# Optimization experiments

Hardware: AMD Instinct MI355X
Metric: run time of the kernel (lower is better)

## Reference

```python
import jax, jax.numpy as jnp
import numpy as np

B, S, E, H, NW, FFN = 16384, 8, 8, 8, 8, 512  # seq==num_heads, embed==n_wires per view() constraint
EPS = 1e-5


def _layer_norm(x, g, b):
    m = x.mean(-1, keepdims=True)
    v = ((x - m) ** 2).mean(-1, keepdims=True)
    return (x - m) / jnp.sqrt(v + EPS) * g + b


def _ring_cnot_z(c):
    # c: [..., NW] = cos(theta) per wire for a product RX state.
    # CNOT(0,1),(1,2),...,(NW-2,NW-1),(NW-1,0) => z_w -> prefix-XOR; Z-expectations factorize:
    # <Z_w> = prod_{j<=w} c_j (w>=1);  <Z_0> = prod_{j>=1} c_j
    cp = jnp.cumprod(c, axis=-1)
    z0 = jnp.prod(c[..., 1:], axis=-1, keepdims=True)
    return jnp.concatenate([z0, cp[..., 1:]], axis=-1)


def setup_inputs() -> dict:
    key = jax.random.key(0)
    ks = jax.random.split(key, 14)
    rn = lambda k, shp, s=0.1: jax.random.normal(k, shp, jnp.float32) * s
    return {
        "x": jax.random.normal(ks[0], (B, S, E), jnp.float32),
        "in_proj_w": rn(ks[1], (3 * E, E)), "in_proj_b": rn(ks[2], (3 * E,)),
        "out_proj_w": rn(ks[3], (E, E)), "out_proj_b": rn(ks[4], (E,)),
        "rx_attn": rn(ks[5], (NW,), 1.0),
        "combine_w": rn(ks[6], (E, E)), "combine_b": rn(ks[7], (E,)),
        "ln1_g": jnp.ones((E,), jnp.float32), "ln1_b": jnp.zeros((E,), jnp.float32),
        "rx_ffn": rn(ks[8], (NW,), 1.0),
        "lin1_w": rn(ks[9], (FFN, NW)), "lin1_b": rn(ks[10], (FFN,)),
        "lin2_w": rn(ks[11], (E, FFN)), "lin2_b": rn(ks[12], (E,)),
        "ln2_g": jnp.ones((E,), jnp.float32), "ln2_b": jnp.zeros((E,), jnp.float32),
    }


def _forward(x, in_proj_w, in_proj_b, out_proj_w, out_proj_b, rx_attn,
             combine_w, combine_b, ln1_g, ln1_b, rx_ffn,
             lin1_w, lin1_b, lin2_w, lin2_b, ln2_g, ln2_b):
    dk = E // H
    # --- nn.MultiheadAttention (self-attn, batch_first, eval/no-dropout) ---
    qkv = x @ in_proj_w.T + in_proj_b                      # [B,S,3E]
    q, k, v = jnp.split(qkv, 3, axis=-1)
    to_h = lambda t: t.reshape(B, S, H, dk).transpose(0, 2, 1, 3)   # [B,H,S,dk]
    scores = jnp.einsum('bhqd,bhkd->bhqk', to_h(q), to_h(k)) / np.float32(np.sqrt(dk))
    a = jax.nn.softmax(scores, axis=-1)
    o = jnp.einsum('bhqk,bhkd->bhqd', a, to_h(v)).transpose(0, 2, 1, 3).reshape(B, S, E)
    attn_out = o @ out_proj_w.T + out_proj_b               # [B,S,E]

    # --- per-head quantum circuit: RX(feature) + RX(param) per wire, CNOT ring, PauliZ ---
    theta = attn_out[:, :H, :NW] + rx_attn                 # head i = seq slot i; feature j -> wire j
    q_out = _ring_cnot_z(jnp.cos(theta)).reshape(B, S, E)  # [B,H,NW] -> [B,S,E]
    q_out = q_out @ combine_w.T + combine_b
    attn_total = (attn_out + q_out) @ combine_w.T + combine_b  # combine applied twice, as in source

    h = _layer_norm(x + attn_total, ln1_g, ln1_b)

    # --- per-token quantum FFN: RX(feature)+RX(param), PauliZ (no entanglers) => cos(theta) ---
    zf = jnp.cos(h[..., :NW] + rx_ffn)                     # [B,S,NW]
    u = jax.nn.relu(zf @ lin1_w.T + lin1_b)                # [B,S,FFN]
    ffn_out = u @ lin2_w.T + lin2_b                        # [B,S,E]

    return _layer_norm(h + ffn_out, ln2_g, ln2_b)


def reference(x, in_proj_w, in_proj_b, out_proj_w, out_proj_b, rx_attn,
              combine_w, combine_b, ln1_g, ln1_b, rx_ffn,
              lin1_w, lin1_b, lin2_w, lin2_b, ln2_g, ln2_b):
    return _forward(x, in_proj_w, in_proj_b, out_proj_w, out_proj_b, rx_attn,
                    combine_w, combine_b, ln1_g, ln1_b, rx_ffn,
                    lin1_w, lin1_b, lin2_w, lin2_b, ln2_g, ln2_b)
```

## Files before the change

### kernel.cpp

```cpp
#include <hip/hip_runtime.h>


typedef __fp16 half2v __attribute__((ext_vector_type(2)));
typedef __fp16 half4  __attribute__((ext_vector_type(4)));
typedef float  float4v __attribute__((ext_vector_type(4)));

#define SWZ(v, J) __int_as_float(__builtin_amdgcn_ds_swizzle(__float_as_int(v), ((J) << 5) | 0x18))
#define SWZ16(v) __int_as_float(__builtin_amdgcn_ds_swizzle(__float_as_int(v), (16 << 10) | 0x1F))
#define DOT8(a, w0, w1)                                                   \
    fmaf((a)[7], (w1).w, fmaf((a)[6], (w1).z, fmaf((a)[5], (w1).y,        \
    fmaf((a)[4], (w1).x, fmaf((a)[3], (w0).w, fmaf((a)[2], (w0).z,        \
    fmaf((a)[1], (w0).y, (a)[0] * (w0).x)))))))

#define O_IPW 0
#define O_OPW 192
#define O_CW  256
#define O_IPB 320
#define O_OPB 344
#define O_CB  352
#define O_RXA 360
#define O_G1  368
#define O_B1  376
#define O_RXF 384
#define O_L2B 392
#define O_G2  400
#define O_B2  408

__global__ __launch_bounds__(256, 2) void tbq_fused(
    const float* __restrict__ x,
    const float* __restrict__ ipw, const float* __restrict__ ipb,
    const float* __restrict__ opw, const float* __restrict__ opb,
    const float* __restrict__ rxa,
    const float* __restrict__ cw,  const float* __restrict__ cb,
    const float* __restrict__ g1,  const float* __restrict__ b1,
    const float* __restrict__ rxf,
    const float* __restrict__ l1w, const float* __restrict__ l1b,
    const float* __restrict__ l2w, const float* __restrict__ l2b,
    const float* __restrict__ g2,  const float* __restrict__ b2,
    float* __restrict__ out)
{
    __shared__ half4 a1l[2048];
    __shared__ half4 a2l[2048];
    __shared__ __align__(16) float lds_hh[256][12];
    __shared__ __align__(16) float wl[416];

    const int tid = threadIdx.x;
    const int l   = tid & 63;
    const int wv  = tid >> 6;
    const int tok = blockIdx.x * 256 + tid;
    const int base = tok * 8;

    const float4* px = reinterpret_cast<const float4*>(x + base);
    float4 xa = px[0], xb = px[1];

    if (tid < 192) wl[O_IPW + tid] = ipw[tid];
    else           wl[O_OPW + (tid - 192)] = opw[tid - 192];
    if (tid < 64)  wl[O_CW + tid] = cw[tid];
    if (tid < 24)  wl[O_IPB + tid] = ipb[tid];
    if (tid < 8) {
        wl[O_OPB + tid] = opb[tid]; wl[O_CB + tid]  = cb[tid];
        wl[O_RXA + tid] = rxa[tid]; wl[O_G1 + tid]  = g1[tid];
        wl[O_B1 + tid]  = b1[tid];  wl[O_RXF + tid] = rxf[tid];
        wl[O_L2B + tid] = l2b[tid]; wl[O_G2 + tid]  = g2[tid];
        wl[O_B2 + tid]  = b2[tid];
    }

    const half4 zh = {(__fp16)0.f, (__fp16)0.f, (__fp16)0.f, (__fp16)0.f};
    #pragma unroll 1
    for (int i = 0; i < 8; ++i) {
        const int u  = tid + i * 256;
        const int nf = u >> 6, ll = u & 63;
        const int mm = ll & 15, kk0 = (ll >> 4) * 4;
        half4 r1 = zh;
        if (ll < 32) {
            float4 w = *reinterpret_cast<const float4*>(l1w + (nf * 16 + mm) * 8 + kk0);
            half2v c0 = __builtin_amdgcn_cvt_pkrtz(w.x, w.y);
            half2v c1 = __builtin_amdgcn_cvt_pkrtz(w.z, w.w);
            r1.x = c0.x; r1.y = c0.y; r1.z = c1.x; r1.w = c1.y;
        } else if (ll < 48) {
            r1.x = (__fp16)l1b[nf * 16 + mm];
        }
        a1l[u] = r1;
        half4 r2 = zh;
        if (mm < 8) {
            float4 w = *reinterpret_cast<const float4*>(l2w + mm * 512 + nf * 16 + kk0);
            half2v c0 = __builtin_amdgcn_cvt_pkrtz(w.x, w.y);
            half2v c1 = __builtin_amdgcn_cvt_pkrtz(w.z, w.w);
            r2.x = c0.x; r2.y = c0.y; r2.z = c1.x; r2.w = c1.y;
        }
        a2l[u] = r2;
    }
    __syncthreads();

    const float4* wl4 = reinterpret_cast<const float4*>(wl);

    float xr[8];
    xr[0] = xa.x; xr[1] = xa.y; xr[2] = xa.z; xr[3] = xa.w;
    xr[4] = xb.x; xr[5] = xb.y; xr[6] = xb.z; xr[7] = xb.w;

    float q[8], k[8], v[8];
    #pragma unroll
    for (int e = 0; e < 8; ++e) {
        float4 wq0 = wl4[e * 2],      wq1 = wl4[e * 2 + 1];
        float4 wk0 = wl4[16 + e * 2], wk1 = wl4[16 + e * 2 + 1];
        float4 wv0 = wl4[32 + e * 2], wv1 = wl4[32 + e * 2 + 1];
        q[e] = wl[O_IPB + e]      + DOT8(xr, wq0, wq1);
        k[e] = wl[O_IPB + 8 + e]  + DOT8(xr, wk0, wk1);
        v[e] = wl[O_IPB + 16 + e] + DOT8(xr, wv0, wv1);
    }

    float orow[8];
    #pragma unroll
    for (int h = 0; h < 8; ++h) {
        const float kh = k[h], vh = v[h];
        const float qh2 = q[h] * 1.44269504f;
        float kk[8], vv[8];
        kk[0] = SWZ(kh, 0); kk[1] = SWZ(kh, 1); kk[2] = SWZ(kh, 2); kk[3] = SWZ(kh, 3);
        kk[4] = SWZ(kh, 4); kk[5] = SWZ(kh, 5); kk[6] = SWZ(kh, 6); kk[7] = SWZ(kh, 7);
        vv[0] = SWZ(vh, 0); vv[1] = SWZ(vh, 1); vv[2] = SWZ(vh, 2); vv[3] = SWZ(vh, 3);
        vv[4] = SWZ(vh, 4); vv[5] = SWZ(vh, 5); vv[6] = SWZ(vh, 6); vv[7] = SWZ(vh, 7);
        float p[8];
        #pragma unroll
        for (int j = 0; j < 8; ++j) p[j] = exp2f(qh2 * kk[j]);
        float sum = ((p[0] + p[1]) + (p[2] + p[3])) + ((p[4] + p[5]) + (p[6] + p[7]));
        float ov = 0.f;
        #pragma unroll
        for (int j = 0; j < 8; ++j) ov = fmaf(p[j], vv[j], ov);
        orow[h] = ov * __builtin_amdgcn_rcpf(sum);
    }

    float ao[8];
    #pragma unroll
    for (int e = 0; e < 8; ++e) {
        float4 wo0 = wl4[48 + e * 2], wo1 = wl4[48 + e * 2 + 1];
        ao[e] = wl[O_OPB + e] + DOT8(orow, wo0, wo1);
    }

    float c[8];
    #pragma unroll
    for (int w = 0; w < 8; ++w) c[w] = __cosf(ao[w] + wl[O_RXA + w]);
    float z[8];
    {
        float run = c[0];
        #pragma unroll
        for (int w = 1; w < 8; ++w) { run *= c[w]; z[w] = run; }
        float s17 = c[1];
        #pragma unroll
        for (int w = 2; w < 8; ++w) s17 *= c[w];
        z[0] = s17;
    }

    float saq[8];
    #pragma unroll
    for (int e = 0; e < 8; ++e) {
        float4 wc0 = wl4[64 + e * 2], wc1 = wl4[64 + e * 2 + 1];
        saq[e] = ao[e] + wl[O_CB + e] + DOT8(z, wc0, wc1);
    }
    float at[8];
    #pragma unroll
    for (int e = 0; e < 8; ++e) {
        float4 wc0 = wl4[64 + e * 2], wc1 = wl4[64 + e * 2 + 1];
        at[e] = wl[O_CB + e] + DOT8(saq, wc0, wc1);
    }

    float r[8]; float mean = 0.f;
    #pragma unroll
    for (int e = 0; e < 8; ++e) { r[e] = xr[e] + at[e]; mean += r[e]; }
    mean *= 0.125f;
    float var = 0.f;
    #pragma unroll
    for (int e = 0; e < 8; ++e) { float d = r[e] - mean; var = fmaf(d, d, var); }
    var *= 0.125f;
    float rs = __builtin_amdgcn_rsqf(var + 1e-5f);
    {
        float4 hlo, hhi;
        hlo.x = fmaf((r[0] - mean) * rs, wl[O_G1 + 0], wl[O_B1 + 0]);
        hlo.y = fmaf((r[1] - mean) * rs, wl[O_G1 + 1], wl[O_B1 + 1]);
        hlo.z = fmaf((r[2] - mean) * rs, wl[O_G1 + 2], wl[O_B1 + 2]);
        hlo.w = fmaf((r[3] - mean) * rs, wl[O_G1 + 3], wl[O_B1 + 3]);
        hhi.x = fmaf((r[4] - mean) * rs, wl[O_G1 + 4], wl[O_B1 + 4]);
        hhi.y = fmaf((r[5] - mean) * rs, wl[O_G1 + 5], wl[O_B1 + 5]);
        hhi.z = fmaf((r[6] - mean) * rs, wl[O_G1 + 6], wl[O_B1 + 6]);
        hhi.w = fmaf((r[7] - mean) * rs, wl[O_G1 + 7], wl[O_B1 + 7]);
        *reinterpret_cast<float4*>(&lds_hh[tid][0]) = hlo;
        *reinterpret_cast<float4*>(&lds_hh[tid][4]) = hhi;
    }

    const int m  = l & 15;
    const int kg = (l >> 4) * 4;
    const int wtok = wv * 64;

    float4 h40 = make_float4(0.f, 0.f, 0.f, 0.f), h41 = h40, h42 = h40, h43 = h40;
    half4 bz0 = zh, bz1 = zh, bz2 = zh, bz3 = zh;
    if (l < 32) {
        h40 = *reinterpret_cast<const float4*>(&lds_hh[wtok + m][kg]);
        h41 = *reinterpret_cast<const float4*>(&lds_hh[wtok + 16 + m][kg]);
        h42 = *reinterpret_cast<const float4*>(&lds_hh[wtok + 32 + m][kg]);
        h43 = *reinterpret_cast<const float4*>(&lds_hh[wtok + 48 + m][kg]);
        float4 rx4 = *reinterpret_cast<const float4*>(&wl[O_RXF + kg]);
        half2v c0, c1;
        c0 = __builtin_amdgcn_cvt_pkrtz(__cosf(h40.x + rx4.x), __cosf(h40.y + rx4.y));
        c1 = __builtin_amdgcn_cvt_pkrtz(__cosf(h40.z + rx4.z), __cosf(h40.w + rx4.w));
        bz0.x = c0.x; bz0.y = c0.y; bz0.z = c1.x; bz0.w = c1.y;
        c0 = __builtin_amdgcn_cvt_pkrtz(__cosf(h41.x + rx4.x), __cosf(h41.y + rx4.y));
        c1 = __builtin_amdgcn_cvt_pkrtz(__cosf(h41.z + rx4.z), __cosf(h41.w + rx4.w));
        bz1.x = c0.x; bz1.y = c0.y; bz1.z = c1.x; bz1.w = c1.y;
        c0 = __builtin_amdgcn_cvt_pkrtz(__cosf(h42.x + rx4.x), __cosf(h42.y + rx4.y));
        c1 = __builtin_amdgcn_cvt_pkrtz(__cosf(h42.z + rx4.z), __cosf(h42.w + rx4.w));
        bz2.x = c0.x; bz2.y = c0.y; bz2.z = c1.x; bz2.w = c1.y;
        c0 = __builtin_amdgcn_cvt_pkrtz(__cosf(h43.x + rx4.x), __cosf(h43.y + rx4.y));
        c1 = __builtin_amdgcn_cvt_pkrtz(__cosf(h43.z + rx4.z), __cosf(h43.w + rx4.w));
        bz3.x = c0.x; bz3.y = c0.y; bz3.z = c1.x; bz3.w = c1.y;
    } else if (l < 48) {
        bz0.x = (__fp16)1.f; bz1.x = (__fp16)1.f;
        bz2.x = (__fp16)1.f; bz3.x = (__fp16)1.f;
    }

    const float4v zero4 = {0.f, 0.f, 0.f, 0.f};
    float4v acc0 = zero4, acc1 = zero4, acc2 = zero4, acc3 = zero4;
    #pragma unroll 2
    for (int nf = 0; nf < 32; ++nf) {
        half4 a1f = a1l[nf * 64 + l];
        half4 a2f = a2l[nf * 64 + l];
        float4v d0 = __builtin_amdgcn_mfma_f32_16x16x16f16(a1f, bz0, zero4, 0, 0, 0);
        float4v d1 = __builtin_amdgcn_mfma_f32_16x16x16f16(a1f, bz1, zero4, 0, 0, 0);
        float4v d2 = __builtin_amdgcn_mfma_f32_16x16x16f16(a1f, bz2, zero4, 0, 0, 0);
        float4v d3 = __builtin_amdgcn_mfma_f32_16x16x16f16(a1f, bz3, zero4, 0, 0, 0);
        half4 bu0, bu1, bu2, bu3;
        {
            half2v p0 = __builtin_amdgcn_cvt_pkrtz(d0.x, d0.y);
            half2v p1 = __builtin_amdgcn_cvt_pkrtz(d0.z, d0.w);
            bu0.x = p0.x; bu0.y = p0.y; bu0.z = p1.x; bu0.w = p1.y;
            p0 = __builtin_amdgcn_cvt_pkrtz(d1.x, d1.y);
            p1 = __builtin_amdgcn_cvt_pkrtz(d1.z, d1.w);
            bu1.x = p0.x; bu1.y = p0.y; bu1.z = p1.x; bu1.w = p1.y;
            p0 = __builtin_amdgcn_cvt_pkrtz(d2.x, d2.y);
            p1 = __builtin_amdgcn_cvt_pkrtz(d2.z, d2.w);
            bu2.x = p0.x; bu2.y = p0.y; bu2.z = p1.x; bu2.w = p1.y;
            p0 = __builtin_amdgcn_cvt_pkrtz(d3.x, d3.y);
            p1 = __builtin_amdgcn_cvt_pkrtz(d3.z, d3.w);
            bu3.x = p0.x; bu3.y = p0.y; bu3.z = p1.x; bu3.w = p1.y;
        }
        bu0 = __builtin_elementwise_max(bu0, zh);
        bu1 = __builtin_elementwise_max(bu1, zh);
        bu2 = __builtin_elementwise_max(bu2, zh);
        bu3 = __builtin_elementwise_max(bu3, zh);
        acc0 = __builtin_amdgcn_mfma_f32_16x16x16f16(a2f, bu0, acc0, 0, 0, 0);
        acc1 = __builtin_amdgcn_mfma_f32_16x16x16f16(a2f, bu1, acc1, 0, 0, 0);
        acc2 = __builtin_amdgcn_mfma_f32_16x16x16f16(a2f, bu2, acc2, 0, 0, 0);
        acc3 = __builtin_amdgcn_mfma_f32_16x16x16f16(a2f, bu3, acc3, 0, 0, 0);
    }

    if (l < 32) {
        const float4 lb4 = *reinterpret_cast<const float4*>(&wl[O_L2B + kg]);
        const float4 g4  = *reinterpret_cast<const float4*>(&wl[O_G2 + kg]);
        const float4 bb4 = *reinterpret_cast<const float4*>(&wl[O_B2 + kg]);
        const int obase = blockIdx.x * 256 + wtok;

        #pragma unroll
        for (int tt = 0; tt < 4; ++tt) {
            float4v acc = (tt == 0) ? acc0 : (tt == 1) ? acc1 : (tt == 2) ? acc2 : acc3;
            float4 h4   = (tt == 0) ? h40  : (tt == 1) ? h41  : (tt == 2) ? h42  : h43;
            float r2[4];
            r2[0] = h4.x + acc.x + lb4.x;
            r2[1] = h4.y + acc.y + lb4.y;
            r2[2] = h4.z + acc.z + lb4.z;
            r2[3] = h4.w + acc.w + lb4.w;
            float part = ((r2[0] + r2[1]) + (r2[2] + r2[3]));
            float mean2 = (part + SWZ16(part)) * 0.125f;
            float d0 = r2[0] - mean2, d1_ = r2[1] - mean2,
                  d2 = r2[2] - mean2, d3 = r2[3] - mean2;
            float vp = ((d0 * d0 + d1_ * d1_) + (d2 * d2 + d3 * d3));
            float rs2 = __builtin_amdgcn_rsqf((vp + SWZ16(vp)) * 0.125f + 1e-5f);
            float4 o;
            o.x = fmaf(d0 * rs2, g4.x, bb4.x);
            o.y = fmaf(d1_ * rs2, g4.y, bb4.y);
            o.z = fmaf(d2 * rs2, g4.z, bb4.z);
            o.w = fmaf(d3 * rs2, g4.w, bb4.w);
            *reinterpret_cast<float4*>(out + (obase + tt * 16 + m) * 8 + kg) = o;
        }
    }
}

extern "C" void kernel_launch(void* const* d_in, const int* in_sizes, int n_in,
                              void* d_out, int out_size, void* d_ws, size_t ws_size,
                              hipStream_t stream) {
    const float* x   = (const float*)d_in[0];
    const float* ipw = (const float*)d_in[1];
    const float* ipb = (const float*)d_in[2];
    const float* opw = (const float*)d_in[3];
    const float* opb = (const float*)d_in[4];
    const float* rxa = (const float*)d_in[5];
    const float* cw  = (const float*)d_in[6];
    const float* cb  = (const float*)d_in[7];
    const float* g1  = (const float*)d_in[8];
    const float* b1  = (const float*)d_in[9];
    const float* rxf = (const float*)d_in[10];
    const float* l1w = (const float*)d_in[11];
    const float* l1b = (const float*)d_in[12];
    const float* l2w = (const float*)d_in[13];
    const float* l2b = (const float*)d_in[14];
    const float* g2  = (const float*)d_in[15];
    const float* b2  = (const float*)d_in[16];
    float* out = (float*)d_out;

    const int tokens = 16384 * 8;
    tbq_fused<<<dim3(tokens / 256), dim3(256), 0, stream>>>(
        x, ipw, ipb, opw, opb, rxa, cw, cb, g1, b1, rxf,
        l1w, l1b, l2w, l2b, g2, b2, out);
}
```

Before: 20.90 us.

## Process two tokens per thread and pack K/V into half2 swizzles

Each block now handles 512 tokens with 256 threads, so every thread processes two tokens. This halves the number of blocks and amortizes the per-block LDS weight staging (fp16 conversion of lin1/lin2) over twice as many tokens, and the FFN MFMA loop reuses each loaded A fragment across 8 token tiles instead of 4. K and V are also packed into one fp16 pair so a single swizzle fetches both, halving cross-lane swizzles in the attention step at the cost of fp16 rounding of K and V. Register pressure rises, so launch bounds drop to one block per SIMD-set, which may reduce occupancy and latency hiding, and there are now only 256 blocks.

```diff
diff --git a/kernel.cpp b/kernel.cpp
--- a/kernel.cpp
+++ b/kernel.cpp
@@ -5,8 +5,8 @@
 typedef __fp16 half4  __attribute__((ext_vector_type(4)));
 typedef float  float4v __attribute__((ext_vector_type(4)));
 
-#define SWZ(v, J) __int_as_float(__builtin_amdgcn_ds_swizzle(__float_as_int(v), ((J) << 5) | 0x18))
 #define SWZ16(v) __int_as_float(__builtin_amdgcn_ds_swizzle(__float_as_int(v), (16 << 10) | 0x1F))
+#define SWZI_(v, dlit) __builtin_amdgcn_ds_swizzle((v), ((dlit) << 5) | 0x18)
 #define DOT8(a, w0, w1)                                                   \
     fmaf((a)[7], (w1).w, fmaf((a)[6], (w1).z, fmaf((a)[5], (w1).y,        \
     fmaf((a)[4], (w1).x, fmaf((a)[3], (w0).w, fmaf((a)[2], (w0).z,        \
@@ -26,7 +26,7 @@
 #define O_G2  400
 #define O_B2  408
 
-__global__ __launch_bounds__(256, 2) void tbq_fused(
+__global__ __launch_bounds__(256, 1) void tbq_fused(
     const float* __restrict__ x,
     const float* __restrict__ ipw, const float* __restrict__ ipb,
     const float* __restrict__ opw, const float* __restrict__ opb,
@@ -41,17 +41,21 @@
 {
     __shared__ half4 a1l[2048];
     __shared__ half4 a2l[2048];
-    __shared__ __align__(16) float lds_hh[256][12];
+    __shared__ __align__(16) float lds_hh[512][12];
     __shared__ __align__(16) float wl[416];
 
     const int tid = threadIdx.x;
     const int l   = tid & 63;
     const int wv  = tid >> 6;
-    const int tok = blockIdx.x * 256 + tid;
-    const int base = tok * 8;
-
-    const float4* px = reinterpret_cast<const float4*>(x + base);
-    float4 xa = px[0], xb = px[1];
+    const int gbase = blockIdx.x * 512;
+
+    float4 xa[2], xb[2];
+    {
+        const float4* p0 = reinterpret_cast<const float4*>(x + (gbase + tid) * 8);
+        const float4* p1 = reinterpret_cast<const float4*>(x + (gbase + 256 + tid) * 8);
+        xa[0] = p0[0]; xb[0] = p0[1];
+        xa[1] = p1[0]; xb[1] = p1[1];
+    }
 
     if (tid < 192) wl[O_IPW + tid] = ipw[tid];
     else           wl[O_OPW + (tid - 192)] = opw[tid - 192];
@@ -94,85 +98,105 @@
 
     const float4* wl4 = reinterpret_cast<const float4*>(wl);
 
-    float xr[8];
-    xr[0] = xa.x; xr[1] = xa.y; xr[2] = xa.z; xr[3] = xa.w;
-    xr[4] = xb.x; xr[5] = xb.y; xr[6] = xb.z; xr[7] = xb.w;
-
-    float q[8], k[8], v[8];
+    float xr[2][8];
+    #pragma unroll
+    for (int s = 0; s < 2; ++s) {
+        xr[s][0] = xa[s].x; xr[s][1] = xa[s].y; xr[s][2] = xa[s].z; xr[s][3] = xa[s].w;
+        xr[s][4] = xb[s].x; xr[s][5] = xb[s].y; xr[s][6] = xb[s].z; xr[s][7] = xb[s].w;
+    }
+
+    float q[2][8], k[2][8], v[2][8];
     #pragma unroll
     for (int e = 0; e < 8; ++e) {
         float4 wq0 = wl4[e * 2],      wq1 = wl4[e * 2 + 1];
         float4 wk0 = wl4[16 + e * 2], wk1 = wl4[16 + e * 2 + 1];
         float4 wv0 = wl4[32 + e * 2], wv1 = wl4[32 + e * 2 + 1];
-        q[e] = wl[O_IPB + e]      + DOT8(xr, wq0, wq1);
-        k[e] = wl[O_IPB + 8 + e]  + DOT8(xr, wk0, wk1);
-        v[e] = wl[O_IPB + 16 + e] + DOT8(xr, wv0, wv1);
-    }
-
-    float orow[8];
+        float bq = wl[O_IPB + e], bk = wl[O_IPB + 8 + e], bv = wl[O_IPB + 16 + e];
+        #pragma unroll
+        for (int s = 0; s < 2; ++s) {
+            q[s][e] = bq + DOT8(xr[s], wq0, wq1);
+            k[s][e] = bk + DOT8(xr[s], wk0, wk1);
+            v[s][e] = bv + DOT8(xr[s], wv0, wv1);
+        }
+    }
+
+    float orow[2][8];
     #pragma unroll
     for (int h = 0; h < 8; ++h) {
-        const float kh = k[h], vh = v[h];
-        const float qh2 = q[h] * 1.44269504f;
-        float kk[8], vv[8];
-        kk[0] = SWZ(kh, 0); kk[1] = SWZ(kh, 1); kk[2] = SWZ(kh, 2); kk[3] = SWZ(kh, 3);
-        kk[4] = SWZ(kh, 4); kk[5] = SWZ(kh, 5); kk[6] = SWZ(kh, 6); kk[7] = SWZ(kh, 7);
-        vv[0] = SWZ(vh, 0); vv[1] = SWZ(vh, 1); vv[2] = SWZ(vh, 2); vv[3] = SWZ(vh, 3);
-        vv[4] = SWZ(vh, 4); vv[5] = SWZ(vh, 5); vv[6] = SWZ(vh, 6); vv[7] = SWZ(vh, 7);
-        float p[8];
-        #pragma unroll
-        for (int j = 0; j < 8; ++j) p[j] = exp2f(qh2 * kk[j]);
-        float sum = ((p[0] + p[1]) + (p[2] + p[3])) + ((p[4] + p[5]) + (p[6] + p[7]));
-        float ov = 0.f;
-        #pragma unroll
-        for (int j = 0; j < 8; ++j) ov = fmaf(p[j], vv[j], ov);
-        orow[h] = ov * __builtin_amdgcn_rcpf(sum);
-    }
-
-    float ao[8];
+        #pragma unroll
+        for (int s = 0; s < 2; ++s) {
+            half2v pk = __builtin_amdgcn_cvt_pkrtz(k[s][h], v[s][h]);
+            int kvp = __builtin_bit_cast(int, pk);
+            int kvg[8];
+            kvg[0] = SWZI_(kvp, 0); kvg[1] = SWZI_(kvp, 1);
+            kvg[2] = SWZI_(kvp, 2); kvg[3] = SWZI_(kvp, 3);
+            kvg[4] = SWZI_(kvp, 4); kvg[5] = SWZI_(kvp, 5);
+            kvg[6] = SWZI_(kvp, 6); kvg[7] = SWZI_(kvp, 7);
+            const float qh2 = q[s][h] * 1.44269504f;
+            float sum = 0.f, ov = 0.f;
+            #pragma unroll
+            for (int j = 0; j < 8; ++j) {
+                half2v kv = __builtin_bit_cast(half2v, kvg[j]);
+                float p = exp2f(qh2 * (float)kv.x);
+                sum += p;
+                ov = fmaf(p, (float)kv.y, ov);
+            }
+            orow[s][h] = ov * __builtin_amdgcn_rcpf(sum);
+        }
+    }
+
+    float ao[2][8];
     #pragma unroll
     for (int e = 0; e < 8; ++e) {
         float4 wo0 = wl4[48 + e * 2], wo1 = wl4[48 + e * 2 + 1];
-        ao[e] = wl[O_OPB + e] + DOT8(orow, wo0, wo1);
-    }
-
-    float c[8];
-    #pragma unroll
-    for (int w = 0; w < 8; ++w) c[w] = __cosf(ao[w] + wl[O_RXA + w]);
-    float z[8];
-    {
+        float bo = wl[O_OPB + e];
+        #pragma unroll
+        for (int s = 0; s < 2; ++s) ao[s][e] = bo + DOT8(orow[s], wo0, wo1);
+    }
+
+    float z[2][8];
+    #pragma unroll
+    for (int s = 0; s < 2; ++s) {
+        float c[8];
+        #pragma unroll
+        for (int w = 0; w < 8; ++w) c[w] = __cosf(ao[s][w] + wl[O_RXA + w]);
         float run = c[0];
         #pragma unroll
-        for (int w = 1; w < 8; ++w) { run *= c[w]; z[w] = run; }
+        for (int w = 1; w < 8; ++w) { run *= c[w]; z[s][w] = run; }
         float s17 = c[1];
         #pragma unroll
         for (int w = 2; w < 8; ++w) s17 *= c[w];
-        z[0] = s17;
-    }
-
-    float saq[8];
+        z[s][0] = s17;
+    }
+
+    float saq[2][8];
     #pragma unroll
     for (int e = 0; e < 8; ++e) {
         float4 wc0 = wl4[64 + e * 2], wc1 = wl4[64 + e * 2 + 1];
-        saq[e] = ao[e] + wl[O_CB + e] + DOT8(z, wc0, wc1);
-    }
-    float at[8];
+        float bc = wl[O_CB + e];
+        #pragma unroll
+        for (int s = 0; s < 2; ++s) saq[s][e] = ao[s][e] + bc + DOT8(z[s], wc0, wc1);
+    }
+    float at[2][8];
     #pragma unroll
     for (int e = 0; e < 8; ++e) {
         float4 wc0 = wl4[64 + e * 2], wc1 = wl4[64 + e * 2 + 1];
-        at[e] = wl[O_CB + e] + DOT8(saq, wc0, wc1);
-    }
-
-    float r[8]; float mean = 0.f;
-    #pragma unroll
-    for (int e = 0; e < 8; ++e) { r[e] = xr[e] + at[e]; mean += r[e]; }
-    mean *= 0.125f;
-    float var = 0.f;
-    #pragma unroll
-    for (int e = 0; e < 8; ++e) { float d = r[e] - mean; var = fmaf(d, d, var); }
-    var *= 0.125f;
-    float rs = __builtin_amdgcn_rsqf(var + 1e-5f);
-    {
+        float bc = wl[O_CB + e];
+        #pragma unroll
+        for (int s = 0; s < 2; ++s) at[s][e] = bc + DOT8(saq[s], wc0, wc1);
+    }
+
+    #pragma unroll
+    for (int s = 0; s < 2; ++s) {
+        float r[8]; float mean = 0.f;
+        #pragma unroll
+        for (int e = 0; e < 8; ++e) { r[e] = xr[s][e] + at[s][e]; mean += r[e]; }
+        mean *= 0.125f;
+        float var = 0.f;
+        #pragma unroll
+        for (int e = 0; e < 8; ++e) { float d = r[e] - mean; var = fmaf(d, d, var); }
+        var *= 0.125f;
+        float rs = __builtin_amdgcn_rsqf(var + 1e-5f);
         float4 hlo, hhi;
         hlo.x = fmaf((r[0] - mean) * rs, wl[O_G1 + 0], wl[O_B1 + 0]);
         hlo.y = fmaf((r[1] - mean) * rs, wl[O_G1 + 1], wl[O_B1 + 1]);
@@ -182,90 +206,67 @@
         hhi.y = fmaf((r[5] - mean) * rs, wl[O_G1 + 5], wl[O_B1 + 5]);
         hhi.z = fmaf((r[6] - mean) * rs, wl[O_G1 + 6], wl[O_B1 + 6]);
         hhi.w = fmaf((r[7] - mean) * rs, wl[O_G1 + 7], wl[O_B1 + 7]);
-        *reinterpret_cast<float4*>(&lds_hh[tid][0]) = hlo;
-        *reinterpret_cast<float4*>(&lds_hh[tid][4]) = hhi;
+        *reinterpret_cast<float4*>(&lds_hh[tid + s * 256][0]) = hlo;
+        *reinterpret_cast<float4*>(&lds_hh[tid + s * 256][4]) = hhi;
     }
 
     const int m  = l & 15;
     const int kg = (l >> 4) * 4;
     const int wtok = wv * 64;
 
-    float4 h40 = make_float4(0.f, 0.f, 0.f, 0.f), h41 = h40, h42 = h40, h43 = h40;
-    half4 bz0 = zh, bz1 = zh, bz2 = zh, bz3 = zh;
+    half4 bz[8];
+    #pragma unroll
+    for (int tt = 0; tt < 8; ++tt) bz[tt] = zh;
     if (l < 32) {
-        h40 = *reinterpret_cast<const float4*>(&lds_hh[wtok + m][kg]);
-        h41 = *reinterpret_cast<const float4*>(&lds_hh[wtok + 16 + m][kg]);
-        h42 = *reinterpret_cast<const float4*>(&lds_hh[wtok + 32 + m][kg]);
-        h43 = *reinterpret_cast<const float4*>(&lds_hh[wtok + 48 + m][kg]);
         float4 rx4 = *reinterpret_cast<const float4*>(&wl[O_RXF + kg]);
-        half2v c0, c1;
-        c0 = __builtin_amdgcn_cvt_pkrtz(__cosf(h40.x + rx4.x), __cosf(h40.y + rx4.y));
-        c1 = __builtin_amdgcn_cvt_pkrtz(__cosf(h40.z + rx4.z), __cosf(h40.w + rx4.w));
-        bz0.x = c0.x; bz0.y = c0.y; bz0.z = c1.x; bz0.w = c1.y;
-        c0 = __builtin_amdgcn_cvt_pkrtz(__cosf(h41.x + rx4.x), __cosf(h41.y + rx4.y));
-        c1 = __builtin_amdgcn_cvt_pkrtz(__cosf(h41.z + rx4.z), __cosf(h41.w + rx4.w));
-        bz1.x = c0.x; bz1.y = c0.y; bz1.z = c1.x; bz1.w = c1.y;
-        c0 = __builtin_amdgcn_cvt_pkrtz(__cosf(h42.x + rx4.x), __cosf(h42.y + rx4.y));
-        c1 = __builtin_amdgcn_cvt_pkrtz(__cosf(h42.z + rx4.z), __cosf(h42.w + rx4.w));
-        bz2.x = c0.x; bz2.y = c0.y; bz2.z = c1.x; bz2.w = c1.y;
-        c0 = __builtin_amdgcn_cvt_pkrtz(__cosf(h43.x + rx4.x), __cosf(h43.y + rx4.y));
-        c1 = __builtin_amdgcn_cvt_pkrtz(__cosf(h43.z + rx4.z), __cosf(h43.w + rx4.w));
-        bz3.x = c0.x; bz3.y = c0.y; bz3.z = c1.x; bz3.w = c1.y;
+        #pragma unroll
+        for (int tt = 0; tt < 8; ++tt) {
+            const int ltok = (tt & 4) * 64 + wtok + (tt & 3) * 16 + m;
+            float4 h4 = *reinterpret_cast<const float4*>(&lds_hh[ltok][kg]);
+            half2v c0 = __builtin_amdgcn_cvt_pkrtz(__cosf(h4.x + rx4.x), __cosf(h4.y + rx4.y));
+            half2v c1 = __builtin_amdgcn_cvt_pkrtz(__cosf(h4.z + rx4.z), __cosf(h4.w + rx4.w));
+            half4 b; b.x = c0.x; b.y = c0.y; b.z = c1.x; b.w = c1.y;
+            bz[tt] = b;
+        }
     } else if (l < 48) {
-        bz0.x = (__fp16)1.f; bz1.x = (__fp16)1.f;
-        bz2.x = (__fp16)1.f; bz3.x = (__fp16)1.f;
+        #pragma unroll
+        for (int tt = 0; tt < 8; ++tt) bz[tt].x = (__fp16)1.f;
     }
 
     const float4v zero4 = {0.f, 0.f, 0.f, 0.f};
-    float4v acc0 = zero4, acc1 = zero4, acc2 = zero4, acc3 = zero4;
+    float4v acc[8];
+    #pragma unroll
+    for (int tt = 0; tt < 8; ++tt) acc[tt] = zero4;
+
     #pragma unroll 2
     for (int nf = 0; nf < 32; ++nf) {
         half4 a1f = a1l[nf * 64 + l];
         half4 a2f = a2l[nf * 64 + l];
-        float4v d0 = __builtin_amdgcn_mfma_f32_16x16x16f16(a1f, bz0, zero4, 0, 0, 0);
-        float4v d1 = __builtin_amdgcn_mfma_f32_16x16x16f16(a1f, bz1, zero4, 0, 0, 0);
-        float4v d2 = __builtin_amdgcn_mfma_f32_16x16x16f16(a1f, bz2, zero4, 0, 0, 0);
-        float4v d3 = __builtin_amdgcn_mfma_f32_16x16x16f16(a1f, bz3, zero4, 0, 0, 0);
-        half4 bu0, bu1, bu2, bu3;
-        {
-            half2v p0 = __builtin_amdgcn_cvt_pkrtz(d0.x, d0.y);
-            half2v p1 = __builtin_amdgcn_cvt_pkrtz(d0.z, d0.w);
-            bu0.x = p0.x; bu0.y = p0.y; bu0.z = p1.x; bu0.w = p1.y;
-            p0 = __builtin_amdgcn_cvt_pkrtz(d1.x, d1.y);
-            p1 = __builtin_amdgcn_cvt_pkrtz(d1.z, d1.w);
-            bu1.x = p0.x; bu1.y = p0.y; bu1.z = p1.x; bu1.w = p1.y;
-            p0 = __builtin_amdgcn_cvt_pkrtz(d2.x, d2.y);
-            p1 = __builtin_amdgcn_cvt_pkrtz(d2.z, d2.w);
-            bu2.x = p0.x; bu2.y = p0.y; bu2.z = p1.x; bu2.w = p1.y;
-            p0 = __builtin_amdgcn_cvt_pkrtz(d3.x, d3.y);
-            p1 = __builtin_amdgcn_cvt_pkrtz(d3.z, d3.w);
-            bu3.x = p0.x; bu3.y = p0.y; bu3.z = p1.x; bu3.w = p1.y;
-        }
-        bu0 = __builtin_elementwise_max(bu0, zh);
-        bu1 = __builtin_elementwise_max(bu1, zh);
-        bu2 = __builtin_elementwise_max(bu2, zh);
-        bu3 = __builtin_elementwise_max(bu3, zh);
-        acc0 = __builtin_amdgcn_mfma_f32_16x16x16f16(a2f, bu0, acc0, 0, 0, 0);
-        acc1 = __builtin_amdgcn_mfma_f32_16x16x16f16(a2f, bu1, acc1, 0, 0, 0);
-        acc2 = __builtin_amdgcn_mfma_f32_16x16x16f16(a2f, bu2, acc2, 0, 0, 0);
-        acc3 = __builtin_amdgcn_mfma_f32_16x16x16f16(a2f, bu3, acc3, 0, 0, 0);
+        #pragma unroll
+        for (int tt = 0; tt < 8; ++tt) {
+            float4v d = __builtin_amdgcn_mfma_f32_16x16x16f16(a1f, bz[tt], zero4, 0, 0, 0);
+            half2v p0 = __builtin_amdgcn_cvt_pkrtz(d.x, d.y);
+            half2v p1 = __builtin_amdgcn_cvt_pkrtz(d.z, d.w);
+            half4 bu; bu.x = p0.x; bu.y = p0.y; bu.z = p1.x; bu.w = p1.y;
+            bu = __builtin_elementwise_max(bu, zh);
+            acc[tt] = __builtin_amdgcn_mfma_f32_16x16x16f16(a2f, bu, acc[tt], 0, 0, 0);
+        }
     }
 
     if (l < 32) {
         const float4 lb4 = *reinterpret_cast<const float4*>(&wl[O_L2B + kg]);
         const float4 g4  = *reinterpret_cast<const float4*>(&wl[O_G2 + kg]);
         const float4 bb4 = *reinterpret_cast<const float4*>(&wl[O_B2 + kg]);
-        const int obase = blockIdx.x * 256 + wtok;
-
-        #pragma unroll
-        for (int tt = 0; tt < 4; ++tt) {
-            float4v acc = (tt == 0) ? acc0 : (tt == 1) ? acc1 : (tt == 2) ? acc2 : acc3;
-            float4 h4   = (tt == 0) ? h40  : (tt == 1) ? h41  : (tt == 2) ? h42  : h43;
+
+        #pragma unroll
+        for (int tt = 0; tt < 8; ++tt) {
+            const int ltok = (tt & 4) * 64 + wtok + (tt & 3) * 16 + m;
+            float4 h4 = *reinterpret_cast<const float4*>(&lds_hh[ltok][kg]);
             float r2[4];
-            r2[0] = h4.x + acc.x + lb4.x;
-            r2[1] = h4.y + acc.y + lb4.y;
-            r2[2] = h4.z + acc.z + lb4.z;
-            r2[3] = h4.w + acc.w + lb4.w;
+            r2[0] = h4.x + acc[tt].x + lb4.x;
+            r2[1] = h4.y + acc[tt].y + lb4.y;
+            r2[2] = h4.z + acc[tt].z + lb4.z;
+            r2[3] = h4.w + acc[tt].w + lb4.w;
             float part = ((r2[0] + r2[1]) + (r2[2] + r2[3]));
             float mean2 = (part + SWZ16(part)) * 0.125f;
             float d0 = r2[0] - mean2, d1_ = r2[1] - mean2,
@@ -277,7 +278,7 @@
             o.y = fmaf(d1_ * rs2, g4.y, bb4.y);
             o.z = fmaf(d2 * rs2, g4.z, bb4.z);
             o.w = fmaf(d3 * rs2, g4.w, bb4.w);
-            *reinterpret_cast<float4*>(out + (obase + tt * 16 + m) * 8 + kg) = o;
+            *reinterpret_cast<float4*>(out + (gbase + ltok) * 8 + kg) = o;
         }
     }
 }
@@ -305,7 +306,7 @@
     float* out = (float*)d_out;
 
     const int tokens = 16384 * 8;
-    tbq_fused<<<dim3(tokens / 256), dim3(256), 0, stream>>>(
+    tbq_fused<<<dim3(tokens / 512), dim3(256), 0, stream>>>(
         x, ipw, ipb, opw, opb, rxa, cw, cb, g1, b1, rxf,
         l1w, l1b, l2w, l2b, g2, b2, out);
 }
```

Result: slower. 24.25 us (+16.0%).

## Hold small projection weights in registers as fp16 and use packed dot2

Applied to the files above, without the earlier changes.

Drops the LDS staging of the in-proj, out-proj and combine weights. Each thread now loads those weights itself, converts them to packed fp16 pairs held in registers, and computes the small 8x8 projections with v_dot2 instructions instead of fp32 FMA chains. K and V are packed into a single 32-bit value so each head's attention needs half as many ds_swizzle ops. This cuts LDS traffic, swizzles and VALU instruction count, at the cost of fp16 precision in the attention path and many more registers, which may hurt occupancy under the 2-blocks-per-CU launch bound.

```diff
diff --git a/kernel.cpp b/kernel.cpp
--- a/kernel.cpp
+++ b/kernel.cpp
@@ -5,26 +5,31 @@
 typedef __fp16 half4  __attribute__((ext_vector_type(4)));
 typedef float  float4v __attribute__((ext_vector_type(4)));
 
-#define SWZ(v, J) __int_as_float(__builtin_amdgcn_ds_swizzle(__float_as_int(v), ((J) << 5) | 0x18))
 #define SWZ16(v) __int_as_float(__builtin_amdgcn_ds_swizzle(__float_as_int(v), (16 << 10) | 0x1F))
-#define DOT8(a, w0, w1)                                                   \
-    fmaf((a)[7], (w1).w, fmaf((a)[6], (w1).z, fmaf((a)[5], (w1).y,        \
-    fmaf((a)[4], (w1).x, fmaf((a)[3], (w0).w, fmaf((a)[2], (w0).z,        \
-    fmaf((a)[1], (w0).y, (a)[0] * (w0).x)))))))
-
-#define O_IPW 0
-#define O_OPW 192
-#define O_CW  256
-#define O_IPB 320
-#define O_OPB 344
-#define O_CB  352
-#define O_RXA 360
-#define O_G1  368
-#define O_B1  376
-#define O_RXF 384
-#define O_L2B 392
-#define O_G2  400
-#define O_B2  408
+#define SWZI_(v, dlit) __builtin_amdgcn_ds_swizzle((v), ((dlit) << 5) | 0x18)
+#define GATHERJ8(dst, src)                                  \
+    do {                                                    \
+        dst[0] = SWZI_(src, 0); dst[1] = SWZI_(src, 1);     \
+        dst[2] = SWZI_(src, 2); dst[3] = SWZI_(src, 3);     \
+        dst[4] = SWZI_(src, 4); dst[5] = SWZI_(src, 5);     \
+        dst[6] = SWZI_(src, 6); dst[7] = SWZI_(src, 7);     \
+    } while (0)
+#define FD4(xv, wr)                                                        \
+    __builtin_amdgcn_fdot2((xv)[3], (wr)[3],                               \
+    __builtin_amdgcn_fdot2((xv)[2], (wr)[2],                               \
+    __builtin_amdgcn_fdot2((xv)[1], (wr)[1],                               \
+    __builtin_amdgcn_fdot2((xv)[0], (wr)[0], 0.f, false), false), false), false)
+
+#define O_IPB 0
+#define O_OPB 24
+#define O_CB  32
+#define O_RXA 40
+#define O_G1  48
+#define O_B1  56
+#define O_RXF 64
+#define O_L2B 72
+#define O_G2  80
+#define O_B2  88
 
 __global__ __launch_bounds__(256, 2) void tbq_fused(
     const float* __restrict__ x,
@@ -42,7 +47,7 @@
     __shared__ half4 a1l[2048];
     __shared__ half4 a2l[2048];
     __shared__ __align__(16) float lds_hh[256][12];
-    __shared__ __align__(16) float wl[416];
+    __shared__ __align__(16) float wl[96];
 
     const int tid = threadIdx.x;
     const int l   = tid & 63;
@@ -53,17 +58,44 @@
     const float4* px = reinterpret_cast<const float4*>(x + base);
     float4 xa = px[0], xb = px[1];
 
-    if (tid < 192) wl[O_IPW + tid] = ipw[tid];
-    else           wl[O_OPW + (tid - 192)] = opw[tid - 192];
-    if (tid < 64)  wl[O_CW + tid] = cw[tid];
-    if (tid < 24)  wl[O_IPB + tid] = ipb[tid];
-    if (tid < 8) {
-        wl[O_OPB + tid] = opb[tid]; wl[O_CB + tid]  = cb[tid];
-        wl[O_RXA + tid] = rxa[tid]; wl[O_G1 + tid]  = g1[tid];
-        wl[O_B1 + tid]  = b1[tid];  wl[O_RXF + tid] = rxf[tid];
-        wl[O_L2B + tid] = l2b[tid]; wl[O_G2 + tid]  = g2[tid];
-        wl[O_B2 + tid]  = b2[tid];
-    }
+    half2v wip[24][4], wop[8][4], wcw[8][4];
+    {
+        const float4* g = reinterpret_cast<const float4*>(ipw);
+        #pragma unroll
+        for (int r = 0; r < 24; ++r) {
+            float4 w0 = g[r * 2], w1 = g[r * 2 + 1];
+            wip[r][0] = __builtin_amdgcn_cvt_pkrtz(w0.x, w0.y);
+            wip[r][1] = __builtin_amdgcn_cvt_pkrtz(w0.z, w0.w);
+            wip[r][2] = __builtin_amdgcn_cvt_pkrtz(w1.x, w1.y);
+            wip[r][3] = __builtin_amdgcn_cvt_pkrtz(w1.z, w1.w);
+        }
+        const float4* go = reinterpret_cast<const float4*>(opw);
+        const float4* gc = reinterpret_cast<const float4*>(cw);
+        #pragma unroll
+        for (int r = 0; r < 8; ++r) {
+            float4 w0 = go[r * 2], w1 = go[r * 2 + 1];
+            wop[r][0] = __builtin_amdgcn_cvt_pkrtz(w0.x, w0.y);
+            wop[r][1] = __builtin_amdgcn_cvt_pkrtz(w0.z, w0.w);
+            wop[r][2] = __builtin_amdgcn_cvt_pkrtz(w1.x, w1.y);
+            wop[r][3] = __builtin_amdgcn_cvt_pkrtz(w1.z, w1.w);
+            float4 c0 = gc[r * 2], c1 = gc[r * 2 + 1];
+            wcw[r][0] = __builtin_amdgcn_cvt_pkrtz(c0.x, c0.y);
+            wcw[r][1] = __builtin_amdgcn_cvt_pkrtz(c0.z, c0.w);
+            wcw[r][2] = __builtin_amdgcn_cvt_pkrtz(c1.x, c1.y);
+            wcw[r][3] = __builtin_amdgcn_cvt_pkrtz(c1.z, c1.w);
+        }
+    }
+
+    if (tid < 24)      wl[O_IPB + tid]        = ipb[tid];
+    else if (tid < 32) wl[O_OPB + (tid - 24)] = opb[tid - 24];
+    else if (tid < 40) wl[O_CB  + (tid - 32)] = cb[tid - 32];
+    else if (tid < 48) wl[O_RXA + (tid - 40)] = rxa[tid - 40];
+    else if (tid < 56) wl[O_G1  + (tid - 48)] = g1[tid - 48];
+    else if (tid < 64) wl[O_B1  + (tid - 56)] = b1[tid - 56];
+    else if (tid < 72) wl[O_RXF + (tid - 64)] = rxf[tid - 64];
+    else if (tid < 80) wl[O_L2B + (tid - 72)] = l2b[tid - 72];
+    else if (tid < 88) wl[O_G2  + (tid - 80)] = g2[tid - 80];
+    else if (tid < 96) wl[O_B2  + (tid - 88)] = b2[tid - 88];
 
     const half4 zh = {(__fp16)0.f, (__fp16)0.f, (__fp16)0.f, (__fp16)0.f};
     #pragma unroll 1
@@ -92,49 +124,51 @@
     }
     __syncthreads();
 
-    const float4* wl4 = reinterpret_cast<const float4*>(wl);
-
     float xr[8];
     xr[0] = xa.x; xr[1] = xa.y; xr[2] = xa.z; xr[3] = xa.w;
     xr[4] = xb.x; xr[5] = xb.y; xr[6] = xb.z; xr[7] = xb.w;
-
-    float q[8], k[8], v[8];
+    half2v xh[4];
+    xh[0] = __builtin_amdgcn_cvt_pkrtz(xr[0], xr[1]);
+    xh[1] = __builtin_amdgcn_cvt_pkrtz(xr[2], xr[3]);
+    xh[2] = __builtin_amdgcn_cvt_pkrtz(xr[4], xr[5]);
+    xh[3] = __builtin_amdgcn_cvt_pkrtz(xr[6], xr[7]);
+
+    float q[8];
+    int kvp[8];
     #pragma unroll
     for (int e = 0; e < 8; ++e) {
-        float4 wq0 = wl4[e * 2],      wq1 = wl4[e * 2 + 1];
-        float4 wk0 = wl4[16 + e * 2], wk1 = wl4[16 + e * 2 + 1];
-        float4 wv0 = wl4[32 + e * 2], wv1 = wl4[32 + e * 2 + 1];
-        q[e] = wl[O_IPB + e]      + DOT8(xr, wq0, wq1);
-        k[e] = wl[O_IPB + 8 + e]  + DOT8(xr, wk0, wk1);
-        v[e] = wl[O_IPB + 16 + e] + DOT8(xr, wv0, wv1);
+        q[e]       = wl[O_IPB + e]      + FD4(xh, wip[e]);
+        float ke   = wl[O_IPB + 8 + e]  + FD4(xh, wip[8 + e]);
+        float ve   = wl[O_IPB + 16 + e] + FD4(xh, wip[16 + e]);
+        half2v pk  = __builtin_amdgcn_cvt_pkrtz(ke, ve);
+        kvp[e] = __builtin_bit_cast(int, pk);
     }
 
     float orow[8];
     #pragma unroll
     for (int h = 0; h < 8; ++h) {
-        const float kh = k[h], vh = v[h];
+        int kvg[8];
+        GATHERJ8(kvg, kvp[h]);
         const float qh2 = q[h] * 1.44269504f;
-        float kk[8], vv[8];
-        kk[0] = SWZ(kh, 0); kk[1] = SWZ(kh, 1); kk[2] = SWZ(kh, 2); kk[3] = SWZ(kh, 3);
-        kk[4] = SWZ(kh, 4); kk[5] = SWZ(kh, 5); kk[6] = SWZ(kh, 6); kk[7] = SWZ(kh, 7);
-        vv[0] = SWZ(vh, 0); vv[1] = SWZ(vh, 1); vv[2] = SWZ(vh, 2); vv[3] = SWZ(vh, 3);
-        vv[4] = SWZ(vh, 4); vv[5] = SWZ(vh, 5); vv[6] = SWZ(vh, 6); vv[7] = SWZ(vh, 7);
-        float p[8];
-        #pragma unroll
-        for (int j = 0; j < 8; ++j) p[j] = exp2f(qh2 * kk[j]);
-        float sum = ((p[0] + p[1]) + (p[2] + p[3])) + ((p[4] + p[5]) + (p[6] + p[7]));
-        float ov = 0.f;
-        #pragma unroll
-        for (int j = 0; j < 8; ++j) ov = fmaf(p[j], vv[j], ov);
+        float sum = 0.f, ov = 0.f;
+        #pragma unroll
+        for (int j = 0; j < 8; ++j) {
+            half2v kv = __builtin_bit_cast(half2v, kvg[j]);
+            float p = exp2f(qh2 * (float)kv.x);
+            sum += p;
+            ov = fmaf(p, (float)kv.y, ov);
+        }
         orow[h] = ov * __builtin_amdgcn_rcpf(sum);
     }
 
+    half2v oh[4];
+    oh[0] = __builtin_amdgcn_cvt_pkrtz(orow[0], orow[1]);
+    oh[1] = __builtin_amdgcn_cvt_pkrtz(orow[2], orow[3]);
+    oh[2] = __builtin_amdgcn_cvt_pkrtz(orow[4], orow[5]);
+    oh[3] = __builtin_amdgcn_cvt_pkrtz(orow[6], orow[7]);
     float ao[8];
     #pragma unroll
-    for (int e = 0; e < 8; ++e) {
-        float4 wo0 = wl4[48 + e * 2], wo1 = wl4[48 + e * 2 + 1];
-        ao[e] = wl[O_OPB + e] + DOT8(orow, wo0, wo1);
-    }
+    for (int e = 0; e < 8; ++e) ao[e] = wl[O_OPB + e] + FD4(oh, wop[e]);
 
     float c[8];
     #pragma unroll
@@ -150,18 +184,23 @@
         z[0] = s17;
     }
 
+    half2v zp[4];
+    zp[0] = __builtin_amdgcn_cvt_pkrtz(z[0], z[1]);
+    zp[1] = __builtin_amdgcn_cvt_pkrtz(z[2], z[3]);
+    zp[2] = __builtin_amdgcn_cvt_pkrtz(z[4], z[5]);
+    zp[3] = __builtin_amdgcn_cvt_pkrtz(z[6], z[7]);
     float saq[8];
     #pragma unroll
-    for (int e = 0; e < 8; ++e) {
-        float4 wc0 = wl4[64 + e * 2], wc1 = wl4[64 + e * 2 + 1];
-        saq[e] = ao[e] + wl[O_CB + e] + DOT8(z, wc0, wc1);
-    }
+    for (int e = 0; e < 8; ++e) saq[e] = ao[e] + wl[O_CB + e] + FD4(zp, wcw[e]);
+
+    half2v sp[4];
+    sp[0] = __builtin_amdgcn_cvt_pkrtz(saq[0], saq[1]);
+    sp[1] = __builtin_amdgcn_cvt_pkrtz(saq[2], saq[3]);
+    sp[2] = __builtin_amdgcn_cvt_pkrtz(saq[4], saq[5]);
+    sp[3] = __builtin_amdgcn_cvt_pkrtz(saq[6], saq[7]);
     float at[8];
     #pragma unroll
-    for (int e = 0; e < 8; ++e) {
-        float4 wc0 = wl4[64 + e * 2], wc1 = wl4[64 + e * 2 + 1];
-        at[e] = wl[O_CB + e] + DOT8(saq, wc0, wc1);
-    }
+    for (int e = 0; e < 8; ++e) at[e] = wl[O_CB + e] + FD4(sp, wcw[e]);
 
     float r[8]; float mean = 0.f;
     #pragma unroll
```

New measurement: 24.29 us. 16.2% more time.
